# Performance work log

Hardware: AMD Instinct MI355X
Metric: run time of the kernel (lower is better)

The kernel has to match this reference:

```python
import jax, jax.numpy as jnp
import numpy as np

NEG_INF = -9e15
ALPHA = 0.2  # LeakyReLU slope
ORDER = 2


def gat_layer(x, adj, W, av, concat=True):
    """GraphAttentionLayer forward (eval mode, dropout off).
    x: (b, f, n, t); adj: (b, n, n) int; W: (b, f, c); av: (b, 2c).
    Equivalent to the original repeat_interleave/repeat construction: the
    einsum of 'a' with the (b, 2c, n, m, t) pairwise tensor is linear, so
    e[b,n,m,t] = leakyrelu(a1.Wh[:,n,t] + a2.Wh[:,m,t]).
    """
    Wh = jnp.einsum('bfnt,bfc->bcnt', x, W)            # (b, c, n, t)
    C = Wh.shape[1]
    f1 = jnp.einsum('bcnt,bc->bnt', Wh, av[:, :C])     # source-node term
    f2 = jnp.einsum('bcnt,bc->bnt', Wh, av[:, C:])     # target-node term
    e = jax.nn.leaky_relu(f1[:, :, None, :] + f2[:, None, :, :], ALPHA)  # (b,n,m,t)
    e = jnp.where(adj[:, :, :, None] > 0, e, NEG_INF)
    att = jax.nn.softmax(e, axis=2)                    # softmax over m
    h = jnp.einsum('bnmt,bcmt->bcnt', att, Wh)
    return jax.nn.elu(h) if concat else h


def setup_inputs() -> dict:
    key = jax.random.key(0)
    ks = jax.random.split(key, 8)
    B, F, N, T = 16, 32, 200, 48
    S = 3  # support_len
    c_out = 64
    c_cat = (ORDER * S + 1) * F  # 224
    x = jax.random.normal(ks[0], (B, F, N, T), dtype=jnp.float32)
    support = jax.random.randint(ks[1], (B, S, N, N), 0, 2, dtype=jnp.int32)
    W1 = jax.random.normal(ks[2], (S, B, F, F), dtype=jnp.float32) * (1.414 / np.sqrt(F))
    a1 = jax.random.normal(ks[3], (S, B, 2 * F), dtype=jnp.float32) * 0.1
    WK = jax.random.normal(ks[4], (S * (ORDER - 1), B, F, F), dtype=jnp.float32) * (1.414 / np.sqrt(F))
    aK = jax.random.normal(ks[5], (S * (ORDER - 1), B, 2 * F), dtype=jnp.float32) * 0.1
    mlp_w = jax.random.normal(ks[6], (c_out, c_cat), dtype=jnp.float32) * (1.0 / np.sqrt(c_cat))
    mlp_b = jnp.zeros((c_out,), dtype=jnp.float32)
    return {"x": x, "support": support, "W1": W1, "a1": a1,
            "WK": WK, "aK": aK, "mlp_w": mlp_w, "mlp_b": mlp_b}


def reference(x, support, W1, a1, WK, aK, mlp_w, mlp_b):
    """gcn3 forward (eval mode): multi-hop GAT diffusion + concat + 1x1 conv."""
    S = support.shape[1]
    out = [x]
    count = 0
    for idx in range(S):
        adj = support[:, idx]
        x1 = gat_layer(x, adj, W1[idx], a1[idx])
        out.append(x1)
        for _ in range(2, ORDER + 1):
            x2 = jax.nn.relu(gat_layer(x1, adj, WK[count], aK[count]))
            out.append(x2)
            x1 = x2
            count += 1
    h = jnp.concatenate(out, axis=1)                    # (b, 7*F, n, t)
    h = jnp.einsum('bcnt,oc->bont', h, mlp_w) + mlp_b[None, :, None, None]
    return h
```

## Files before the change

### kernel.cpp

```cpp
#include <hip/hip_runtime.h>
#include <math.h>

#define BB 16
#define FD 32
#define ND 200
#define TD 48
#define SD 3
#define OC 64
#define SLICE 6400
#define TSTRIDE 4915200
#define NEGBIG (-9.0e15f)
#define LOG2E 1.44269504088896340736f

typedef __attribute__((ext_vector_type(8))) short bf16x8;
typedef __attribute__((ext_vector_type(4))) float f32x4;
typedef __attribute__((ext_vector_type(4))) unsigned int u32x4;

static __device__ __forceinline__ unsigned short f2bf(float f) {
  unsigned u = __builtin_bit_cast(unsigned, f);
  return (unsigned short)((u + 0x8000u) >> 16);
}
static __device__ __forceinline__ unsigned short f2bf_rne(float f) {
  unsigned u = __builtin_bit_cast(unsigned, f);
  return (unsigned short)((u + 0x7FFFu + ((u >> 16) & 1u)) >> 16);
}
static __device__ __forceinline__ float bf2f(unsigned short h) {
  unsigned u = ((unsigned)h) << 16;
  return __builtin_bit_cast(float, u);
}

static __device__ __forceinline__ unsigned int pk_bf16_rhu(float a, float b) {
  unsigned ua = __builtin_bit_cast(unsigned, a) + 0x8000u;
  unsigned ub = __builtin_bit_cast(unsigned, b) + 0x8000u;
#if __has_builtin(__builtin_amdgcn_perm)
  return __builtin_amdgcn_perm(ub, ua, 0x07060302u);
#else
  return (ua >> 16) | (ub & 0xFFFF0000u);
#endif
}

#if __has_builtin(__builtin_amdgcn_exp2f)
static __device__ __forceinline__ float exp2_hw(float x) { return __builtin_amdgcn_exp2f(x); }
#else
static __device__ __forceinline__ float exp2_hw(float x) { return exp2f(x); }
#endif

#if __has_builtin(__builtin_amdgcn_rcpf)
static __device__ __forceinline__ float rcp_hw(float x) { return __builtin_amdgcn_rcpf(x); }
#else
static __device__ __forceinline__ float rcp_hw(float x) { return 1.0f / x; }
#endif

static __device__ __forceinline__ unsigned int sext_bit(unsigned int v, int j) {
#if __has_builtin(__builtin_amdgcn_sbfe)
  return (unsigned int)__builtin_amdgcn_sbfe((int)v, j, 1);
#else
  return 0u - ((v >> j) & 1u);
#endif
}

static __device__ __forceinline__ unsigned int merge_hw(unsigned int lo, unsigned int hi) {
#if __has_builtin(__builtin_amdgcn_perm)
  return __builtin_amdgcn_perm(hi, lo, 0x07060100u);
#else
  return (lo & 0x0000FFFFu) | (hi & 0xFFFF0000u);
#endif
}

__global__ __launch_bounds__(256) void k_prep(
    const float* __restrict__ x, const int* __restrict__ support,
    const float* __restrict__ W1, const float* __restrict__ WK,
    const float* __restrict__ a1, const float* __restrict__ aK,
    const float* __restrict__ mw,
    unsigned short* __restrict__ Xtnc, unsigned short* __restrict__ Xntc,
    unsigned long long* __restrict__ msk,
    unsigned short* __restrict__ Wtb, unsigned short* __restrict__ Wxb,
    unsigned short* __restrict__ mwb) {
  __shared__ float sbuf[3104];
  int bid = blockIdx.x;
  if (bid < 800) {
    int b = bid / 50, n0 = (bid % 50) * 4;
    unsigned short* sf16 = (unsigned short*)sbuf;
    const float4* xv = (const float4*)x;
    for (int i = threadIdx.x; i < 1536; i += 256) {
      int nn = i / 384, rem = i % 384, f = rem / 12, q = rem % 12;
      float4 v = xv[(size_t)((b * 32 + f) * ND + n0 + nn) * 12 + q];
      unsigned short* p = &sf16[f * 194 + nn * 48 + 4 * q];
      p[0] = f2bf(v.x);
      p[1] = f2bf(v.y);
      p[2] = f2bf(v.z);
      p[3] = f2bf(v.w);
    }
    __syncthreads();
    unsigned int* dt = (unsigned int*)Xtnc;
    unsigned int* dn = (unsigned int*)Xntc;
    for (int j = threadIdx.x; j < 3072; j += 256) {
      int t = j >> 6, rem = j & 63, nn = rem >> 4, fq = rem & 15;
      int col = nn * 48 + t;
      unsigned int v = (unsigned int)sf16[(2 * fq) * 194 + col] |
                       ((unsigned int)sf16[(2 * fq + 1) * 194 + col] << 16);
      dt[((size_t)(b * 48 + t) * ND + n0 + nn) * 16 + fq] = v;
    }
    for (int j = threadIdx.x; j < 3072; j += 256) {
      int nn = j / 768, rem = j % 768, t = rem >> 4, fq = rem & 15;
      int col = nn * 48 + t;
      unsigned int v = (unsigned int)sf16[(2 * fq) * 194 + col] |
                       ((unsigned int)sf16[(2 * fq + 1) * 194 + col] << 16);
      dn[((size_t)(b * ND + n0 + nn) * 48 + t) * 16 + fq] = v;
    }
  } else if (bid < 1424) {
    int q = bid - 800;
    int si = q / 13, rg = q % 13;
    const int* adjb = support + (size_t)si * ND * ND;
    int wv = threadIdx.x >> 6, lane = threadIdx.x & 63;
#pragma unroll
    for (int j = 0; j < 4; j++) {
      int r = rg * 16 + wv * 4 + j;
      unsigned long long ws0 = 0, ws1 = 0, ws2 = 0, ws3 = 0;
      if (r < ND) {
        ws0 = __ballot(adjb[r * ND + lane] > 0);
        ws1 = __ballot(adjb[r * ND + 64 + lane] > 0);
        ws2 = __ballot(((128 + lane < ND) ? adjb[r * ND + 128 + lane] : 0) > 0);
        ws3 = __ballot(((192 + lane < ND) ? adjb[r * ND + 192 + lane] : 0) > 0);
      }
      if (lane < 4 && r < 208) {
        unsigned long long o = 0;
#pragma unroll
        for (int k = 0; k < 7; k++) {
          int bidx = k * 4 + lane;
          int sel = bidx >> 3;
          unsigned long long src = (sel == 0) ? ws0 : (sel == 1) ? ws1
                                 : (sel == 2) ? ws2 : ws3;
          unsigned long long byte = (src >> ((bidx & 7) * 8)) & 0xFFull;
          o |= byte << (8 * k);
        }
        msk[((size_t)si * 208 + r) * 4 + lane] = o;
      }
    }
  } else {
    int b2 = bid - 1424;
    if (b2 < 96) {
      int mat = b2 >> 4, b = b2 & 15;
      const float* src = (mat < 3) ? (W1 + (size_t)(mat * 16 + b) * 1024)
                                   : (WK + (size_t)((mat - 3) * 16 + b) * 1024);
      const float* av = (mat < 3) ? (a1 + (size_t)mat * 1024 + b * 64)
                                  : (aK + (size_t)(mat - 3) * 1024 + b * 64);
      unsigned short* dst = Wtb + (size_t)b2 * 1024;
      for (int i = threadIdx.x; i < 1024; i += 256) {
        int c = i >> 5, f = i & 31;
        dst[c * 32 + f] = f2bf_rne(src[f * 32 + c]);
      }
      if (threadIdx.x < 32) {
        int f = threadIdx.x;
        float s1 = 0.f, s2 = 0.f;
        for (int c = 0; c < 32; c++) {
          float wfc = src[f * 32 + c];
          s1 = fmaf(wfc, av[c], s1);
          s2 = fmaf(wfc, av[32 + c], s2);
        }
        sbuf[f] = s1;
        sbuf[32 + f] = s2;
      }
      __syncthreads();
      unsigned short* wx = Wxb + (size_t)b2 * 512;
      for (int i = threadIdx.x; i < 512; i += 256) {
        int col = i >> 5, f = i & 31;
        unsigned short o = 0;
        if (col < 4) {
          float s = sbuf[(col >> 1) * 32 + f];
          unsigned short hi = f2bf_rne(s);
          o = (col & 1) ? f2bf_rne(s - bf2f(hi)) : hi;
        }
        wx[i] = o;
      }
    } else {
      int i = (b2 - 96) * 256 + threadIdx.x;
      if (i < OC * 224) mwb[i] = f2bf_rne(mw[i]);
    }
  }
}

__global__ __launch_bounds__(256) void k_gat2(
    const unsigned short* __restrict__ Xb,
    const unsigned short* __restrict__ Wtb,
    const unsigned short* __restrict__ Wxb,
    const unsigned char* __restrict__ mskb,
    unsigned short* __restrict__ bfp) {
  int bx = blockIdx.x;
  int idx = bx / (BB * TD);
  int bt = bx % (BB * TD);
  int b = bt / TD, t = bt % TD;
  __shared__ __align__(16) unsigned short Vt[32 * 232];
  __shared__ __align__(16) unsigned short Y1s[208 * 32];
  __shared__ __align__(16) unsigned int f2e[224];
  __shared__ __align__(16) float2 f1e[208];
  __shared__ float SVa[64];
  int tid = threadIdx.x, w = tid >> 6, lane = tid & 63;
  int cl = lane & 15, qd = lane >> 4;

  if (tid < 64) SVa[tid] = 0.f;
  for (int i = tid; i < 512; i += 256) {
    int cch = i >> 4, d = i & 15;
    ((unsigned int*)&Vt[cch * 232 + 200])[d] = 0u;
  }
  for (int i = tid; i < 128; i += 256)
    ((unsigned int*)&Y1s[200 * 32])[i] = 0u;
  __syncthreads();

  const unsigned char* mrow = mskb + (size_t)(b * SD + idx) * 208 * 32;
  bf16x8 ones;
#pragma unroll
  for (int j = 0; j < 8; j++) ones[j] = (short)0x3F80;
  size_t xbase = (size_t)bt * SLICE;
  unsigned short* Yb1 = bfp + (size_t)(1 + 2 * idx) * TSTRIDE;
  unsigned short* Yb2 = bfp + (size_t)(2 + 2 * idx) * TSTRIDE;
  const float C1 = LOG2E;
  const float C2 = 0.2f * LOG2E;

#pragma unroll
  for (int hop = 0; hop < 2; hop++) {
    int mat = (hop == 0) ? idx : (3 + idx);
    const unsigned short* wtb = Wtb + (size_t)(mat * 16 + b) * 1024;
    const unsigned short* wxb = Wxb + (size_t)(mat * 16 + b) * 512;
    bf16x8 Bw0 = *(const bf16x8*)(wtb + cl * 32 + qd * 8);
    bf16x8 Bw1 = *(const bf16x8*)(wtb + (cl + 16) * 32 + qd * 8);
    bf16x8 Bwx = *(const bf16x8*)(wxb + cl * 32 + qd * 8);
    float* SV = SVa + hop * 32;

    for (int ti = w; ti < 13; ti += 4) {
      bf16x8 A;
      if (hop == 0)
        A = *(const bf16x8*)(Xb + xbase + (size_t)(ti * 16 + cl) * 32 + qd * 8);
      else
        A = *(const bf16x8*)&Y1s[(ti * 16 + cl) * 32 + qd * 8];
      f32x4 d0 = {0.f, 0.f, 0.f, 0.f}, d1 = d0, d2 = d0;
      d0 = __builtin_amdgcn_mfma_f32_16x16x32_bf16(A, Bw0, d0, 0, 0, 0);
      d1 = __builtin_amdgcn_mfma_f32_16x16x32_bf16(A, Bw1, d1, 0, 0, 0);
      d2 = __builtin_amdgcn_mfma_f32_16x16x32_bf16(A, Bwx, d2, 0, 0, 0);
      int rn0 = ti * 16 + qd * 4;
      float s0 = 0.f, s1 = 0.f;
#pragma unroll
      for (int r = 0; r < 4; r++) {
        float fv = d2[r] + __shfl_xor(d2[r], 1, 64);
        int rn = rn0 + r;
        if (rn < ND) {
          s0 += d0[r];
          s1 += d1[r];
          float E = exp2_hw(fv * C1);
          float Es = exp2_hw(fv * C2);
          if (cl == 0) f1e[rn] = make_float2(E, Es);
          if (cl == 2) f2e[rn] = pk_bf16_rhu(Es, E);
        }
      }
      if (rn0 + 3 < ND) {
        uint2 q0, q1;
        q0.x = pk_bf16_rhu(d0[0], d0[1]);
        q0.y = pk_bf16_rhu(d0[2], d0[3]);
        q1.x = pk_bf16_rhu(d1[0], d1[1]);
        q1.y = pk_bf16_rhu(d1[2], d1[3]);
        *(uint2*)&Vt[cl * 232 + rn0] = q0;
        *(uint2*)&Vt[(cl + 16) * 232 + rn0] = q1;
      }
      atomicAdd(&SV[cl], s0);
      atomicAdd(&SV[cl + 16], s1);
    }
    __syncthreads();

    for (int ti = w; ti < 13; ti += 4) {
      int row = ti * 16 + cl;
      float2 e1p = f1e[row];
      float E1 = e1p.x, E1s = e1p.y;
      const unsigned long long mq =
          *(const unsigned long long*)(mrow + (size_t)row * 32 + qd * 8);
      f32x4 denom = {0.f, 0.f, 0.f, 0.f};
      f32x4 acc0 = denom, acc1 = denom;
#pragma unroll
      for (int k = 0; k < 7; k++) {
        int m0 = k * 32 + qd * 8;
        bf16x8 b0 = *(const bf16x8*)&Vt[cl * 232 + m0];
        bf16x8 b1 = *(const bf16x8*)&Vt[(cl + 16) * 232 + m0];
        u32x4 ua = *(const u32x4*)&f2e[m0];
        u32x4 ub = *(const u32x4*)&f2e[m0 + 4];
        unsigned int mby = (unsigned int)(mq >> (8 * k)) & 0xFFu;
        u32x4 aw;
#pragma unroll
        for (int p = 0; p < 4; p++) {
          unsigned int u0 = (p < 2) ? ((p & 1) ? ua.z : ua.x)
                                    : ((p & 1) ? ub.z : ub.x);
          unsigned int u1 = (p < 2) ? ((p & 1) ? ua.w : ua.y)
                                    : ((p & 1) ? ub.w : ub.y);
          float p0 = fmaxf(E1 * __builtin_bit_cast(float, u0 & 0xFFFF0000u),
                           E1s * __builtin_bit_cast(float, u0 << 16));
          float p1 = fmaxf(E1 * __builtin_bit_cast(float, u1 & 0xFFFF0000u),
                           E1s * __builtin_bit_cast(float, u1 << 16));
          unsigned int pk = pk_bf16_rhu(p0, p1);
          unsigned int mlo = sext_bit(mby, 2 * p);
          unsigned int mhi = sext_bit(mby, 2 * p + 1);
          aw[p] = pk & merge_hw(mlo, mhi);
        }
        bf16x8 A = __builtin_bit_cast(bf16x8, aw);
        denom = __builtin_amdgcn_mfma_f32_16x16x32_bf16(A, ones, denom, 0, 0, 0);
        acc0 = __builtin_amdgcn_mfma_f32_16x16x32_bf16(A, b0, acc0, 0, 0, 0);
        acc1 = __builtin_amdgcn_mfma_f32_16x16x32_bf16(A, b1, acc1, 0, 0, 0);
      }
#pragma unroll
      for (int r = 0; r < 4; r++) {
        int rn = ti * 16 + qd * 4 + r;
        if (rn < ND) {
          float dn = denom[r];
          float v0, v1;
          if (dn > 0.f) {
            float iv = rcp_hw(dn);
            v0 = acc0[r] * iv;
            v1 = acc1[r] * iv;
          } else {
            v0 = SV[cl] * (1.0f / ND);
            v1 = SV[cl + 16] * (1.0f / ND);
          }
          if (hop == 0) {
            v0 = (v0 > 0.f) ? v0 : exp2_hw(v0 * LOG2E) - 1.f;
            v1 = (v1 > 0.f) ? v1 : exp2_hw(v1 * LOG2E) - 1.f;
          } else {
            v0 = fmaxf(v0, 0.f);
            v1 = fmaxf(v1, 0.f);
          }
          Y1s[rn * 32 + cl] = f2bf(v0);
          Y1s[rn * 32 + cl + 16] = f2bf(v1);
        }
      }
    }
    __syncthreads();
    {
      unsigned short* Yb = (hop == 0) ? Yb1 : Yb2;
      for (int i = tid; i < 800; i += 256) {
        int rn = i >> 2, part = i & 3;
        uint4 vq = *(const uint4*)&Y1s[rn * 32 + part * 8];
        *(uint4*)(Yb + ((size_t)(b * ND + rn) * TD + t) * 32 + part * 8) = vq;
      }
    }
  }
}

__global__ __launch_bounds__(256) void k_conv(
    const unsigned short* __restrict__ hb,
    const unsigned short* __restrict__ mwb,
    const float* __restrict__ mb,
    float* __restrict__ out) {
  int bn = blockIdx.x;
  int b = bn / 100, n0 = (bn % 100) * 2;
  int w = threadIdx.x >> 6, lane = threadIdx.x & 63;
  int cl = lane & 15, qd = lane >> 4;
  bf16x8 bw[7];
#pragma unroll
  for (int k = 0; k < 7; k++)
    bw[k] = *(const bf16x8*)(mwb + (size_t)(w * 16 + cl) * 224 + k * 32 + qd * 8);
  int o = w * 16 + cl;
  float bias = mb[o];
#pragma unroll
  for (int nn = 0; nn < 2; nn++) {
    int n = n0 + nn;
#pragma unroll
    for (int mt = 0; mt < 3; mt++) {
      size_t abase = ((size_t)(b * ND + n) * TD + mt * 16 + cl) * 32 + qd * 8;
      f32x4 acc = {0.f, 0.f, 0.f, 0.f};
#pragma unroll
      for (int k = 0; k < 7; k++) {
        bf16x8 A = *(const bf16x8*)(hb + (size_t)k * TSTRIDE + abase);
        acc = __builtin_amdgcn_mfma_f32_16x16x32_bf16(A, bw[k], acc, 0, 0, 0);
      }
      float4 st;
      st.x = acc[0] + bias;
      st.y = acc[1] + bias;
      st.z = acc[2] + bias;
      st.w = acc[3] + bias;
      *(float4*)(out + ((size_t)(b * OC + o) * ND + n) * TD + mt * 16 + qd * 4) = st;
    }
  }
}

extern "C" void kernel_launch(void* const* d_in, const int* in_sizes, int n_in,
                              void* d_out, int out_size, void* d_ws, size_t ws_size,
                              hipStream_t stream) {
  const float* x = (const float*)d_in[0];
  const int* support = (const int*)d_in[1];
  const float* W1 = (const float*)d_in[2];
  const float* a1 = (const float*)d_in[3];
  const float* WK = (const float*)d_in[4];
  const float* aK = (const float*)d_in[5];
  const float* mw = (const float*)d_in[6];
  const float* mb = (const float*)d_in[7];
  float* out = (float*)d_out;
  char* wsb = (char*)d_ws;
  unsigned short* Xbt = (unsigned short*)wsb;
  unsigned short* bfp = (unsigned short*)(wsb + 9831424);
  unsigned char* msk = (unsigned char*)(wsb + 78644224);
  unsigned short* mwb = (unsigned short*)(wsb + 78963712);
  unsigned short* Wtb = (unsigned short*)(wsb + 78992384);
  unsigned short* Wxb = (unsigned short*)(wsb + 79188992);

  k_prep<<<1576, 256, 0, stream>>>(x, support, W1, WK, a1, aK, mw, Xbt, bfp,
                                   (unsigned long long*)msk, Wtb, Wxb, mwb);
  k_gat2<<<SD * BB * TD, 256, 0, stream>>>(Xbt, Wtb, Wxb, msk, bfp);
  k_conv<<<BB * 100, 256, 0, stream>>>(bfp, mwb, mb, out);
}
```

Before: 238.8 us.

## Process two time steps per GAT block to reuse mask and weights

Each k_gat2 block now handles two consecutive time steps instead of one, and the grid is halved. The per-row adjacency mask load, mask expansion and weight fragment loads are shared between the two steps, and the MFMA chains for the two steps are interleaved so they can issue alongside each other. Shared memory doubles to about 46KB per block and register pressure rises, which may cut occupancy, and fewer blocks (1152) are available to fill the GPU.

Result: slower. 302.5 us (+26.7%).

```diff
diff --git a/kernel.cpp b/kernel.cpp
--- a/kernel.cpp
+++ b/kernel.cpp
@@ -187,31 +187,36 @@
     const unsigned char* __restrict__ mskb,
     unsigned short* __restrict__ bfp) {
   int bx = blockIdx.x;
-  int idx = bx / (BB * TD);
-  int bt = bx % (BB * TD);
-  int b = bt / TD, t = bt % TD;
-  __shared__ __align__(16) unsigned short Vt[32 * 232];
-  __shared__ __align__(16) unsigned short Y1s[208 * 32];
-  __shared__ __align__(16) unsigned int f2e[224];
-  __shared__ __align__(16) float2 f1e[208];
-  __shared__ float SVa[64];
+  int idx = bx / (BB * 24);
+  int rem = bx % (BB * 24);
+  int b = rem / 24, tq = rem % 24;
+  int t0 = tq * 2;
+  int bt0 = b * TD + t0;
+  __shared__ __align__(16) unsigned short Vt[2][32 * 232];
+  __shared__ __align__(16) unsigned short Y1s[2][208 * 32];
+  __shared__ __align__(16) unsigned int f2e[2][224];
+  __shared__ __align__(16) float2 f1e[2][208];
+  __shared__ float SVa[2][64];
   int tid = threadIdx.x, w = tid >> 6, lane = tid & 63;
   int cl = lane & 15, qd = lane >> 4;
 
-  if (tid < 64) SVa[tid] = 0.f;
-  for (int i = tid; i < 512; i += 256) {
-    int cch = i >> 4, d = i & 15;
-    ((unsigned int*)&Vt[cch * 232 + 200])[d] = 0u;
+  if (tid < 128) ((float*)SVa)[tid] = 0.f;
+  for (int i = tid; i < 1024; i += 256) {
+    int tt = i >> 9, j = i & 511;
+    int cch = j >> 4, d = j & 15;
+    ((unsigned int*)&Vt[tt][cch * 232 + 200])[d] = 0u;
   }
-  for (int i = tid; i < 128; i += 256)
-    ((unsigned int*)&Y1s[200 * 32])[i] = 0u;
+  {
+    int i = tid;
+    int tt = i >> 7, j = i & 127;
+    ((unsigned int*)&Y1s[tt][200 * 32])[j] = 0u;
+  }
   __syncthreads();
 
   const unsigned char* mrow = mskb + (size_t)(b * SD + idx) * 208 * 32;
   bf16x8 ones;
 #pragma unroll
   for (int j = 0; j < 8; j++) ones[j] = (short)0x3F80;
-  size_t xbase = (size_t)bt * SLICE;
   unsigned short* Yb1 = bfp + (size_t)(1 + 2 * idx) * TSTRIDE;
   unsigned short* Yb2 = bfp + (size_t)(2 + 2 * idx) * TSTRIDE;
   const float C1 = LOG2E;
@@ -225,118 +230,166 @@
     bf16x8 Bw0 = *(const bf16x8*)(wtb + cl * 32 + qd * 8);
     bf16x8 Bw1 = *(const bf16x8*)(wtb + (cl + 16) * 32 + qd * 8);
     bf16x8 Bwx = *(const bf16x8*)(wxb + cl * 32 + qd * 8);
-    float* SV = SVa + hop * 32;
 
     for (int ti = w; ti < 13; ti += 4) {
-      bf16x8 A;
-      if (hop == 0)
-        A = *(const bf16x8*)(Xb + xbase + (size_t)(ti * 16 + cl) * 32 + qd * 8);
-      else
-        A = *(const bf16x8*)&Y1s[(ti * 16 + cl) * 32 + qd * 8];
-      f32x4 d0 = {0.f, 0.f, 0.f, 0.f}, d1 = d0, d2 = d0;
-      d0 = __builtin_amdgcn_mfma_f32_16x16x32_bf16(A, Bw0, d0, 0, 0, 0);
-      d1 = __builtin_amdgcn_mfma_f32_16x16x32_bf16(A, Bw1, d1, 0, 0, 0);
-      d2 = __builtin_amdgcn_mfma_f32_16x16x32_bf16(A, Bwx, d2, 0, 0, 0);
+      int roff = (ti * 16 + cl) * 32 + qd * 8;
+      bf16x8 Aa, Ab;
+      if (hop == 0) {
+        Aa = *(const bf16x8*)(Xb + (size_t)bt0 * SLICE + roff);
+        Ab = *(const bf16x8*)(Xb + (size_t)(bt0 + 1) * SLICE + roff);
+      } else {
+        Aa = *(const bf16x8*)&Y1s[0][roff];
+        Ab = *(const bf16x8*)&Y1s[1][roff];
+      }
+      f32x4 z = {0.f, 0.f, 0.f, 0.f};
+      f32x4 d0a = z, d1a = z, d2a = z, d0b = z, d1b = z, d2b = z;
+      d0a = __builtin_amdgcn_mfma_f32_16x16x32_bf16(Aa, Bw0, d0a, 0, 0, 0);
+      d0b = __builtin_amdgcn_mfma_f32_16x16x32_bf16(Ab, Bw0, d0b, 0, 0, 0);
+      d1a = __builtin_amdgcn_mfma_f32_16x16x32_bf16(Aa, Bw1, d1a, 0, 0, 0);
+      d1b = __builtin_amdgcn_mfma_f32_16x16x32_bf16(Ab, Bw1, d1b, 0, 0, 0);
+      d2a = __builtin_amdgcn_mfma_f32_16x16x32_bf16(Aa, Bwx, d2a, 0, 0, 0);
+      d2b = __builtin_amdgcn_mfma_f32_16x16x32_bf16(Ab, Bwx, d2b, 0, 0, 0);
       int rn0 = ti * 16 + qd * 4;
-      float s0 = 0.f, s1 = 0.f;
+      float s0a = 0.f, s1a = 0.f, s0b = 0.f, s1b = 0.f;
 #pragma unroll
       for (int r = 0; r < 4; r++) {
-        float fv = d2[r] + __shfl_xor(d2[r], 1, 64);
+        float fva = d2a[r] + __shfl_xor(d2a[r], 1, 64);
+        float fvb = d2b[r] + __shfl_xor(d2b[r], 1, 64);
         int rn = rn0 + r;
         if (rn < ND) {
-          s0 += d0[r];
-          s1 += d1[r];
-          float E = exp2_hw(fv * C1);
-          float Es = exp2_hw(fv * C2);
-          if (cl == 0) f1e[rn] = make_float2(E, Es);
-          if (cl == 2) f2e[rn] = pk_bf16_rhu(Es, E);
+          s0a += d0a[r];
+          s1a += d1a[r];
+          s0b += d0b[r];
+          s1b += d1b[r];
+          float Ea = exp2_hw(fva * C1), Esa = exp2_hw(fva * C2);
+          float Eb = exp2_hw(fvb * C1), Esb = exp2_hw(fvb * C2);
+          if (cl == 0) {
+            f1e[0][rn] = make_float2(Ea, Esa);
+            f1e[1][rn] = make_float2(Eb, Esb);
+          }
+          if (cl == 2) {
+            f2e[0][rn] = pk_bf16_rhu(Esa, Ea);
+            f2e[1][rn] = pk_bf16_rhu(Esb, Eb);
+          }
         }
       }
       if (rn0 + 3 < ND) {
         uint2 q0, q1;
-        q0.x = pk_bf16_rhu(d0[0], d0[1]);
-        q0.y = pk_bf16_rhu(d0[2], d0[3]);
-        q1.x = pk_bf16_rhu(d1[0], d1[1]);
-        q1.y = pk_bf16_rhu(d1[2], d1[3]);
-        *(uint2*)&Vt[cl * 232 + rn0] = q0;
-        *(uint2*)&Vt[(cl + 16) * 232 + rn0] = q1;
-      }
-      atomicAdd(&SV[cl], s0);
-      atomicAdd(&SV[cl + 16], s1);
+        q0.x = pk_bf16_rhu(d0a[0], d0a[1]);
+        q0.y = pk_bf16_rhu(d0a[2], d0a[3]);
+        q1.x = pk_bf16_rhu(d1a[0], d1a[1]);
+        q1.y = pk_bf16_rhu(d1a[2], d1a[3]);
+        *(uint2*)&Vt[0][cl * 232 + rn0] = q0;
+        *(uint2*)&Vt[0][(cl + 16) * 232 + rn0] = q1;
+        q0.x = pk_bf16_rhu(d0b[0], d0b[1]);
+        q0.y = pk_bf16_rhu(d0b[2], d0b[3]);
+        q1.x = pk_bf16_rhu(d1b[0], d1b[1]);
+        q1.y = pk_bf16_rhu(d1b[2], d1b[3]);
+        *(uint2*)&Vt[1][cl * 232 + rn0] = q0;
+        *(uint2*)&Vt[1][(cl + 16) * 232 + rn0] = q1;
+      }
+      atomicAdd(&SVa[0][hop * 32 + cl], s0a);
+      atomicAdd(&SVa[0][hop * 32 + cl + 16], s1a);
+      atomicAdd(&SVa[1][hop * 32 + cl], s0b);
+      atomicAdd(&SVa[1][hop * 32 + cl + 16], s1b);
     }
     __syncthreads();
 
     for (int ti = w; ti < 13; ti += 4) {
       int row = ti * 16 + cl;
-      float2 e1p = f1e[row];
-      float E1 = e1p.x, E1s = e1p.y;
+      float2 e1a = f1e[0][row], e1b = f1e[1][row];
+      float E1a = e1a.x, E1sa = e1a.y, E1b = e1b.x, E1sb = e1b.y;
       const unsigned long long mq =
           *(const unsigned long long*)(mrow + (size_t)row * 32 + qd * 8);
-      f32x4 denom = {0.f, 0.f, 0.f, 0.f};
-      f32x4 acc0 = denom, acc1 = denom;
+      f32x4 z = {0.f, 0.f, 0.f, 0.f};
+      f32x4 dena = z, a0a = z, a1a = z, denb = z, a0b = z, a1b = z;
 #pragma unroll
       for (int k = 0; k < 7; k++) {
         int m0 = k * 32 + qd * 8;
-        bf16x8 b0 = *(const bf16x8*)&Vt[cl * 232 + m0];
-        bf16x8 b1 = *(const bf16x8*)&Vt[(cl + 16) * 232 + m0];
-        u32x4 ua = *(const u32x4*)&f2e[m0];
-        u32x4 ub = *(const u32x4*)&f2e[m0 + 4];
+        bf16x8 b0a = *(const bf16x8*)&Vt[0][cl * 232 + m0];
+        bf16x8 b1a = *(const bf16x8*)&Vt[0][(cl + 16) * 232 + m0];
+        bf16x8 b0b = *(const bf16x8*)&Vt[1][cl * 232 + m0];
+        bf16x8 b1b = *(const bf16x8*)&Vt[1][(cl + 16) * 232 + m0];
+        u32x4 uaa = *(const u32x4*)&f2e[0][m0];
+        u32x4 uba = *(const u32x4*)&f2e[0][m0 + 4];
+        u32x4 uab = *(const u32x4*)&f2e[1][m0];
+        u32x4 ubb = *(const u32x4*)&f2e[1][m0 + 4];
         unsigned int mby = (unsigned int)(mq >> (8 * k)) & 0xFFu;
-        u32x4 aw;
+        u32x4 awa, awb;
 #pragma unroll
         for (int p = 0; p < 4; p++) {
-          unsigned int u0 = (p < 2) ? ((p & 1) ? ua.z : ua.x)
-                                    : ((p & 1) ? ub.z : ub.x);
-          unsigned int u1 = (p < 2) ? ((p & 1) ? ua.w : ua.y)
-                                    : ((p & 1) ? ub.w : ub.y);
-          float p0 = fmaxf(E1 * __builtin_bit_cast(float, u0 & 0xFFFF0000u),
-                           E1s * __builtin_bit_cast(float, u0 << 16));
-          float p1 = fmaxf(E1 * __builtin_bit_cast(float, u1 & 0xFFFF0000u),
-                           E1s * __builtin_bit_cast(float, u1 << 16));
-          unsigned int pk = pk_bf16_rhu(p0, p1);
           unsigned int mlo = sext_bit(mby, 2 * p);
           unsigned int mhi = sext_bit(mby, 2 * p + 1);
-          aw[p] = pk & merge_hw(mlo, mhi);
-        }
-        bf16x8 A = __builtin_bit_cast(bf16x8, aw);
-        denom = __builtin_amdgcn_mfma_f32_16x16x32_bf16(A, ones, denom, 0, 0, 0);
-        acc0 = __builtin_amdgcn_mfma_f32_16x16x32_bf16(A, b0, acc0, 0, 0, 0);
-        acc1 = __builtin_amdgcn_mfma_f32_16x16x32_bf16(A, b1, acc1, 0, 0, 0);
+          unsigned int mm = merge_hw(mlo, mhi);
+          unsigned int u0 = (p < 2) ? ((p & 1) ? uaa.z : uaa.x)
+                                    : ((p & 1) ? uba.z : uba.x);
+          unsigned int u1 = (p < 2) ? ((p & 1) ? uaa.w : uaa.y)
+                                    : ((p & 1) ? uba.w : uba.y);
+          float p0 = fmaxf(E1a * __builtin_bit_cast(float, u0 & 0xFFFF0000u),
+                           E1sa * __builtin_bit_cast(float, u0 << 16));
+          float p1 = fmaxf(E1a * __builtin_bit_cast(float, u1 & 0xFFFF0000u),
+                           E1sa * __builtin_bit_cast(float, u1 << 16));
+          awa[p] = pk_bf16_rhu(p0, p1) & mm;
+          unsigned int v0 = (p < 2) ? ((p & 1) ? uab.z : uab.x)
+                                    : ((p & 1) ? ubb.z : ubb.x);
+          unsigned int v1 = (p < 2) ? ((p & 1) ? uab.w : uab.y)
+                                    : ((p & 1) ? ubb.w : ubb.y);
+          float q0 = fmaxf(E1b * __builtin_bit_cast(float, v0 & 0xFFFF0000u),
+                           E1sb * __builtin_bit_cast(float, v0 << 16));
+          float q1 = fmaxf(E1b * __builtin_bit_cast(float, v1 & 0xFFFF0000u),
+                           E1sb * __builtin_bit_cast(float, v1 << 16));
+          awb[p] = pk_bf16_rhu(q0, q1) & mm;
+        }
+        bf16x8 Aa = __builtin_bit_cast(bf16x8, awa);
+        bf16x8 Ab = __builtin_bit_cast(bf16x8, awb);
+        dena = __builtin_amdgcn_mfma_f32_16x16x32_bf16(Aa, ones, dena, 0, 0, 0);
+        denb = __builtin_amdgcn_mfma_f32_16x16x32_bf16(Ab, ones, denb, 0, 0, 0);
+        a0a = __builtin_amdgcn_mfma_f32_16x16x32_bf16(Aa, b0a, a0a, 0, 0, 0);
+        a0b = __builtin_amdgcn_mfma_f32_16x16x32_bf16(Ab, b0b, a0b, 0, 0, 0);
+        a1a = __builtin_amdgcn_mfma_f32_16x16x32_bf16(Aa, b1a, a1a, 0, 0, 0);
+        a1b = __builtin_amdgcn_mfma_f32_16x16x32_bf16(Ab, b1b, a1b, 0, 0, 0);
       }
 #pragma unroll
       for (int r = 0; r < 4; r++) {
         int rn = ti * 16 + qd * 4 + r;
         if (rn < ND) {
-          float dn = denom[r];
-          float v0, v1;
-          if (dn > 0.f) {
-            float iv = rcp_hw(dn);
-            v0 = acc0[r] * iv;
-            v1 = acc1[r] * iv;
-          } else {
-            v0 = SV[cl] * (1.0f / ND);
-            v1 = SV[cl + 16] * (1.0f / ND);
+#pragma unroll
+          for (int tt = 0; tt < 2; tt++) {
+            float dn = tt ? denb[r] : dena[r];
+            float x0 = tt ? a0b[r] : a0a[r];
+            float x1 = tt ? a1b[r] : a1a[r];
+            float v0, v1;
+            if (dn > 0.f) {
+              float iv = rcp_hw(dn);
+              v0 = x0 * iv;
+              v1 = x1 * iv;
+            } else {
+              v0 = SVa[tt][hop * 32 + cl] * (1.0f / ND);
+              v1 = SVa[tt][hop * 32 + cl + 16] * (1.0f / ND);
+            }
+            if (hop == 0) {
+              v0 = (v0 > 0.f) ? v0 : exp2_hw(v0 * LOG2E) - 1.f;
+              v1 = (v1 > 0.f) ? v1 : exp2_hw(v1 * LOG2E) - 1.f;
+            } else {
+              v0 = fmaxf(v0, 0.f);
+              v1 = fmaxf(v1, 0.f);
+            }
+            Y1s[tt][rn * 32 + cl] = f2bf(v0);
+            Y1s[tt][rn * 32 + cl + 16] = f2bf(v1);
           }
-          if (hop == 0) {
-            v0 = (v0 > 0.f) ? v0 : exp2_hw(v0 * LOG2E) - 1.f;
-            v1 = (v1 > 0.f) ? v1 : exp2_hw(v1 * LOG2E) - 1.f;
-          } else {
-            v0 = fmaxf(v0, 0.f);
-            v1 = fmaxf(v1, 0.f);
-          }
-          Y1s[rn * 32 + cl] = f2bf(v0);
-          Y1s[rn * 32 + cl + 16] = f2bf(v1);
         }
       }
     }
     __syncthreads();
     {
       unsigned short* Yb = (hop == 0) ? Yb1 : Yb2;
-      for (int i = tid; i < 800; i += 256) {
-        int rn = i >> 2, part = i & 3;
-        uint4 vq = *(const uint4*)&Y1s[rn * 32 + part * 8];
-        *(uint4*)(Yb + ((size_t)(b * ND + rn) * TD + t) * 32 + part * 8) = vq;
-      }
+#pragma unroll
+      for (int tt = 0; tt < 2; tt++)
+        for (int i = tid; i < 800; i += 256) {
+          int rn = i >> 2, part = i & 3;
+          uint4 vq = *(const uint4*)&Y1s[tt][rn * 32 + part * 8];
+          *(uint4*)(Yb + ((size_t)(b * ND + rn) * TD + t0 + tt) * 32 + part * 8) = vq;
+        }
     }
   }
 }
@@ -400,6 +453,6 @@
 
   k_prep<<<1576, 256, 0, stream>>>(x, support, W1, WK, a1, aK, mw, Xbt, bfp,
                                    (unsigned long long*)msk, Wtb, Wxb, mwb);
-  k_gat2<<<SD * BB * TD, 256, 0, stream>>>(Xbt, Wtb, Wxb, msk, bfp);
+  k_gat2<<<SD * BB * (TD / 2), 256, 0, stream>>>(Xbt, Wtb, Wxb, msk, bfp);
   k_conv<<<BB * 100, 256, 0, stream>>>(bfp, mwb, mb, out);
 }
```
